# Kernel tuning notes

Measured on AMD Instinct MI355X. Metric: run time of the kernel, lower is better.

The kernel has to match this reference:

```python
import jax, jax.numpy as jnp
import numpy as np

N_NODES = 25000
N_EDGES = 250000
F_IN = 32
F_OUT = 32
EDGE_DIM = 6
H1, H2 = 64, 128


def setup_inputs() -> dict:
    key = jax.random.key(0)
    ks = jax.random.split(key, 10)
    s = 0.05
    return {
        "x": jax.random.normal(ks[0], (N_NODES, F_IN), dtype=jnp.float32),
        "edge_attr": jax.random.normal(ks[1], (N_EDGES, EDGE_DIM), dtype=jnp.float32),
        # fnet MLP params: Linear(6->64), ReLU, Linear(64->128), ReLU, Linear(128->F_IN*F_OUT)
        "W1": jax.random.normal(ks[2], (H1, EDGE_DIM), dtype=jnp.float32) * s,
        "b1": jnp.zeros((H1,), dtype=jnp.float32),
        "W2": jax.random.normal(ks[3], (H2, H1), dtype=jnp.float32) * s,
        "b2": jnp.zeros((H2,), dtype=jnp.float32),
        "W3": jax.random.normal(ks[4], (F_IN * F_OUT, H2), dtype=jnp.float32) * s,
        "b3": jnp.zeros((F_IN * F_OUT,), dtype=jnp.float32),
        "edge_src": jax.random.randint(ks[5], (N_EDGES,), 0, N_NODES),
        "edge_dst": jax.random.randint(ks[6], (N_EDGES,), 0, N_NODES),
    }


def reference(x, edge_attr, W1, b1, W2, b2, W3, b3, edge_src, edge_dst):
    # fnet: per-edge MLP producing a dynamic filter theta_e of shape [F_OUT, F_IN]
    h = jax.nn.relu(edge_attr @ W1.T + b1)            # [E, H1]
    h = jax.nn.relu(h @ W2.T + b2)                    # [E, H2]
    theta = (h @ W3.T + b3).reshape(-1, F_OUT, F_IN)  # [E, F_OUT, F_IN]
    # gather source features, apply per-edge filter
    msg = jnp.einsum('eoi,ei->eo', theta, x[edge_src])  # [E, F_OUT]
    # scatter-mean over destination nodes (ECC averages over neighborhood)
    agg = jax.ops.segment_sum(msg, edge_dst, num_segments=N_NODES)
    deg = jax.ops.segment_sum(jnp.ones((msg.shape[0],), x.dtype), edge_dst,
                              num_segments=N_NODES)
    out = agg / jnp.maximum(deg, 1.0)[:, None]        # [N, F_OUT]
    return jax.nn.relu(out)                           # trailing 'r' in config
```

## Files before the change

### kernel.cpp

```cpp
#include <hip/hip_runtime.h>
#include <hip/hip_fp16.h>

#define N_NODES 25000
#define N_EDGES 250000
#define ED 6
#define H1 64
#define H2 128
#define NBLK 977
#define NCHUNK 33
#define CHUNK_USH 4096
#define W3S_USHORTS (NCHUNK*CHUNK_USH)
#define W2S_USHORTS (H2*H1)
#define SCAN_BLOCKS 98

typedef float f32x4 __attribute__((ext_vector_type(4)));
typedef _Float16 f16x8 __attribute__((ext_vector_type(8)));
typedef _Float16 f16x2 __attribute__((ext_vector_type(2)));
typedef __fp16 fp16x2 __attribute__((ext_vector_type(2)));
typedef unsigned int u32x4 __attribute__((ext_vector_type(4)));
typedef unsigned int u32x2 __attribute__((ext_vector_type(2)));

union F16x8U { u32x4 u; f16x8 h; };
union F16x2U { unsigned u; f16x2 h; };
union PKU    { fp16x2 p; unsigned u; };

__device__ __forceinline__ unsigned pkrtz(float lo, float hi) {
    PKU r; r.p = __builtin_amdgcn_cvt_pkrtz(lo, hi); return r.u;
}
__device__ __forceinline__ unsigned pk_mul_blo(unsigned h, unsigned x) {
    unsigned d;
    asm("v_pk_mul_f16 %0, %1, %2 op_sel:[0,0] op_sel_hi:[0,1]" : "=v"(d) : "v"(h), "v"(x));
    return d;
}
__device__ __forceinline__ unsigned pk_mul_bhi(unsigned h, unsigned x) {
    unsigned d;
    asm("v_pk_mul_f16 %0, %1, %2 op_sel:[1,0] op_sel_hi:[1,1]" : "=v"(d) : "v"(h), "v"(x));
    return d;
}
__device__ __forceinline__ f32x4 mfma16(f16x8 a, f16x8 b, f32x4 c) {
    return __builtin_amdgcn_mfma_f32_16x16x32_f16(a, b, c, 0, 0, 0);
}
__device__ __forceinline__ void gload16(const void* g, void* l) {
    __builtin_amdgcn_global_load_lds(
        (const __attribute__((address_space(1))) unsigned int*)g,
        (__attribute__((address_space(3))) unsigned int*)l, 16, 0, 0);
}

__global__ __launch_bounds__(256) void ecc_init(
    const float* __restrict__ W3, const float* __restrict__ b3,
    const float* __restrict__ W2,
    unsigned* __restrict__ cnt, unsigned short* __restrict__ w3s,
    unsigned short* __restrict__ w2s)
{
    int idx = blockIdx.x * 256 + threadIdx.x;
    if (idx < W3S_USHORTS) {
        int c = idx >> 12, r = idx & 4095;
        int kk = r >> 10;
        int j  = (r >> 9) & 1;
        int lane = (r >> 3) & 63;
        int m  = r & 7;
        int p  = j * 16 + (lane & 15);
        int o  = ((p & 15) << 1) + (p >> 4);
        int kp = (c * 4 + kk) * 32 + (lane >> 4) * 8 + m;
        float v = 0.f;
        if (kp < 4096)      { int k = kp >> 5, i = kp & 31; v = W3[(o * 32 + i) * 128 + k]; }
        else if (kp < 4128) { v = b3[o * 32 + (kp - 4096)]; }
        __half hv = __float2half_rn(v);
        w3s[idx] = *reinterpret_cast<unsigned short*>(&hv);
    }
    if (idx < W2S_USHORTS) {
        __half hv = __float2half_rn(W2[idx]);
        w2s[idx] = *reinterpret_cast<unsigned short*>(&hv);
    }
    if (idx < N_NODES) cnt[idx] = 0u;
}

__global__ __launch_bounds__(256) void ecc_hist(
    const int* __restrict__ dst, unsigned* __restrict__ cnt,
    unsigned* __restrict__ rank)
{
    int e = blockIdx.x * 256 + threadIdx.x;
    if (e < N_EDGES) rank[e] = atomicAdd(&cnt[dst[e]], 1u);
}

__global__ __launch_bounds__(256) void ecc_scan1(
    const unsigned* __restrict__ cnt, unsigned* __restrict__ off,
    unsigned* __restrict__ bsum)
{
    __shared__ unsigned s[256];
    const int t = threadIdx.x, i = blockIdx.x * 256 + t;
    unsigned v = (i < N_NODES) ? cnt[i] : 0u;
    s[t] = v; __syncthreads();
    #pragma unroll
    for (int d = 1; d < 256; d <<= 1) {
        unsigned add = (t >= d) ? s[t - d] : 0u;
        __syncthreads(); s[t] += add; __syncthreads();
    }
    if (i < N_NODES) off[i] = s[t] - v;
    if (t == 255) bsum[blockIdx.x] = s[255];
}

__global__ __launch_bounds__(128) void ecc_scan2(
    const unsigned* __restrict__ bsum, unsigned* __restrict__ bsumx)
{
    __shared__ unsigned s[128];
    const int t = threadIdx.x;
    unsigned v = (t < SCAN_BLOCKS) ? bsum[t] : 0u;
    s[t] = v; __syncthreads();
    #pragma unroll
    for (int d = 1; d < 128; d <<= 1) {
        unsigned add = (t >= d) ? s[t - d] : 0u;
        __syncthreads(); s[t] += add; __syncthreads();
    }
    if (t < SCAN_BLOCKS) bsumx[t] = s[t] - v;
}

__global__ __launch_bounds__(256) void ecc_scan3(
    unsigned* __restrict__ off, const unsigned* __restrict__ bsumx)
{
    int i = blockIdx.x * 256 + threadIdx.x;
    if (i < N_NODES) off[i] += bsumx[blockIdx.x];
    if (i == 0) off[N_NODES] = N_EDGES;
}

__global__ __launch_bounds__(256) void ecc_perm(
    const int* __restrict__ dst, const unsigned* __restrict__ off,
    const unsigned* __restrict__ rank, unsigned* __restrict__ perm)
{
    int e = blockIdx.x * 256 + threadIdx.x;
    if (e < N_EDGES) perm[off[dst[e]] + rank[e]] = (unsigned)e;
}

__global__ __launch_bounds__(256)
__attribute__((amdgpu_waves_per_eu(2, 2)))
void ecc_fused(
    const float* __restrict__ x,   const float* __restrict__ ea,
    const float* __restrict__ W1,  const float* __restrict__ b1,
    const unsigned short* __restrict__ w2s, const float* __restrict__ b2,
    const unsigned short* __restrict__ w3s,
    const int* __restrict__ src,   const unsigned* __restrict__ perm,
    unsigned* __restrict__ msg32)
{
    __shared__ __align__(16) unsigned short sm[256 * H2];
    __shared__ __align__(16) unsigned short wbuf[2][CHUNK_USH];

    const int t = threadIdx.x;
    const int tile = blockIdx.x * 256;
    const int slot = tile + t;
    const bool ev = (slot < N_EDGES);
    const unsigned je = ev ? perm[slot] : 0u;

    const int w = t >> 6, l = t & 63, lr = l & 15, kg = l >> 4;

    gload16(w3s + t * 8,        &wbuf[0][t * 8]);
    gload16(w3s + 2048 + t * 8, &wbuf[0][2048 + t * 8]);

    {
        float a[ED];
        #pragma unroll
        for (int c = 0; c < ED; ++c) a[c] = ev ? ea[(long)je * ED + c] : 0.f;

        float h1[H1];
        #pragma unroll
        for (int o = 0; o < H1; ++o) {
            float acc = b1[o];
            #pragma unroll
            for (int c = 0; c < ED; ++c) acc = fmaf(W1[o * ED + c], a[c], acc);
            h1[o] = fmaxf(acc, 0.f);
        }
        #pragma unroll
        for (int q = 0; q < 8; ++q) {
            u32x4 pk;
            #pragma unroll
            for (int j = 0; j < 4; ++j)
                pk[j] = pkrtz(h1[q*8 + 2*j], h1[q*8 + 2*j + 1]);
            const int boff = (t * 128 + q * 16) ^ ((t & 7) << 4);
            *(u32x4*)((char*)sm + boff) = pk;
        }
    }

    unsigned xsh[4][4];
    #pragma unroll
    for (int mt = 0; mt < 4; ++mt) {
        const int er = tile + w * 64 + mt * 16 + lr;
        if (er < N_EDGES) {
            const float4* xp = (const float4*)(x + (long)src[perm[er]] * 32 + kg * 8);
            float4 v0 = xp[0], v1 = xp[1];
            xsh[mt][0] = pkrtz(v0.x, v0.y); xsh[mt][1] = pkrtz(v0.z, v0.w);
            xsh[mt][2] = pkrtz(v1.x, v1.y); xsh[mt][3] = pkrtz(v1.z, v1.w);
        } else {
            xsh[mt][0] = xsh[mt][1] = xsh[mt][2] = xsh[mt][3] = 0u;
        }
    }

    {
        F16x8U hb[4][2];
        #pragma unroll
        for (int ne = 0; ne < 4; ++ne) {
            const int er = w * 64 + ne * 16 + lr;
            #pragma unroll
            for (int ks = 0; ks < 2; ++ks) {
                const int boff = (er * 128 + ks * 64 + kg * 16) ^ ((er & 7) << 4);
                hb[ne][ks].u = *(const u32x4*)((const char*)sm + boff);
            }
        }
        __syncthreads();

        #pragma unroll
        for (int mo = 0; mo < 8; ++mo) {
            F16x8U a2[2];
            #pragma unroll
            for (int ks = 0; ks < 2; ++ks)
                a2[ks].u = *(const u32x4*)(w2s + (mo*16 + lr) * 64 + ks*32 + kg*8);
            const float4 bv = *(const float4*)(b2 + mo*16 + kg*4);
            #pragma unroll
            for (int ne = 0; ne < 4; ++ne) {
                f32x4 c = (f32x4){0.f, 0.f, 0.f, 0.f};
                c = mfma16(a2[0].h, hb[ne][0].h, c);
                c = mfma16(a2[1].h, hb[ne][1].h, c);
                const unsigned p0 = pkrtz(fmaxf(c[0]+bv.x, 0.f), fmaxf(c[1]+bv.y, 0.f));
                const unsigned p1 = pkrtz(fmaxf(c[2]+bv.z, 0.f), fmaxf(c[3]+bv.w, 0.f));
                const int er = w * 64 + ne * 16 + lr;
                const int boff = (er * 256 + (mo*16 + kg*4) * 2) ^ ((er & 7) << 4);
                *(u32x2*)((char*)sm + boff) = (u32x2){p0, p1};
            }
        }
    }

    f32x4 acc[4][2];
    #pragma unroll
    for (int mt = 0; mt < 4; ++mt)
        #pragma unroll
        for (int nt = 0; nt < 2; ++nt) acc[mt][nt] = (f32x4){0.f,0.f,0.f,0.f};

    __syncthreads();

    int cur = 0;
    #pragma unroll 1
    for (int c = 0; c < 32; ++c) {
        {
            const unsigned short* gs = w3s + (c + 1) * CHUNK_USH + t * 8;
            gload16(gs,        &wbuf[cur ^ 1][t * 8]);
            gload16(gs + 2048, &wbuf[cur ^ 1][2048 + t * 8]);
        }
        const char* wb = (const char*)wbuf[cur] + l * 16;

        u32x2 hv[4];
        #pragma unroll
        for (int mt = 0; mt < 4; ++mt) {
            const int row = w * 64 + mt * 16 + lr;
            const int boff = (row * 256 + c * 8) ^ ((row & 7) << 4);
            hv[mt] = *(const u32x2*)((const char*)sm + boff);
        }
        #pragma unroll
        for (int kk = 0; kk < 4; ++kk) {
            F16x8U b0, b1;
            b0.u = *(const u32x4*)(wb + kk * 2048);
            b1.u = *(const u32x4*)(wb + kk * 2048 + 1024);
            #pragma unroll
            for (int mt = 0; mt < 4; ++mt) {
                const unsigned h01 = hv[mt][kk >> 1];
                F16x8U af;
                if (kk & 1) {
                    af.u[0] = pk_mul_bhi(h01, xsh[mt][0]);
                    af.u[1] = pk_mul_bhi(h01, xsh[mt][1]);
                    af.u[2] = pk_mul_bhi(h01, xsh[mt][2]);
                    af.u[3] = pk_mul_bhi(h01, xsh[mt][3]);
                } else {
                    af.u[0] = pk_mul_blo(h01, xsh[mt][0]);
                    af.u[1] = pk_mul_blo(h01, xsh[mt][1]);
                    af.u[2] = pk_mul_blo(h01, xsh[mt][2]);
                    af.u[3] = pk_mul_blo(h01, xsh[mt][3]);
                }
                acc[mt][0] = mfma16(af.h, b0.h, acc[mt][0]);
                acc[mt][1] = mfma16(af.h, b1.h, acc[mt][1]);
            }
        }
        __syncthreads();
        cur ^= 1;
    }
    {
        const char* wb = (const char*)wbuf[cur] + l * 16;
        F16x8U b0, b1;
        b0.u = *(const u32x4*)(wb);
        b1.u = *(const u32x4*)(wb + 1024);
        #pragma unroll
        for (int mt = 0; mt < 4; ++mt) {
            F16x8U af;
            af.u = (u32x4){xsh[mt][0], xsh[mt][1], xsh[mt][2], xsh[mt][3]};
            acc[mt][0] = mfma16(af.h, b0.h, acc[mt][0]);
            acc[mt][1] = mfma16(af.h, b1.h, acc[mt][1]);
        }
    }

    #pragma unroll
    for (int mt = 0; mt < 4; ++mt) {
        #pragma unroll
        for (int r = 0; r < 4; ++r) {
            const int j = tile + w * 64 + mt * 16 + kg * 4 + r;
            if (j < N_EDGES)
                msg32[(long)j * 16 + lr] = pkrtz(acc[mt][0][r], acc[mt][1][r]);
        }
    }
}

__global__ __launch_bounds__(256) void ecc_gather(
    const unsigned* __restrict__ msg32, const unsigned* __restrict__ off,
    float* __restrict__ out)
{
    const int t = threadIdx.x;
    const int q = t & 15;
    const int n = blockIdx.x * 16 + (t >> 4);
    if (n >= N_NODES) return;
    const unsigned lo = off[n], hi = off[n + 1];
    float s0 = 0.f, s1 = 0.f;
    for (unsigned j = lo; j < hi; ++j) {
        F16x2U v; v.u = msg32[(long)j * 16 + q];
        s0 += (float)v.h[0];
        s1 += (float)v.h[1];
    }
    const float dg = fmaxf((float)(hi - lo), 1.f);
    ((float2*)(out + (long)n * 32))[q] =
        make_float2(fmaxf(s0 / dg, 0.f), fmaxf(s1 / dg, 0.f));
}

extern "C" void kernel_launch(void* const* d_in, const int* in_sizes, int n_in,
                              void* d_out, int out_size, void* d_ws, size_t ws_size,
                              hipStream_t stream) {
    const float* x   = (const float*)d_in[0];
    const float* ea  = (const float*)d_in[1];
    const float* W1  = (const float*)d_in[2];
    const float* b1  = (const float*)d_in[3];
    const float* W2  = (const float*)d_in[4];
    const float* b2  = (const float*)d_in[5];
    const float* W3  = (const float*)d_in[6];
    const float* b3  = (const float*)d_in[7];
    const int*   src = (const int*)d_in[8];
    const int*   dst = (const int*)d_in[9];
    float* out = (float*)d_out;

    char* p = (char*)d_ws;
    unsigned short* w3s = (unsigned short*)p; p += W3S_USHORTS * 2;
    unsigned short* w2s = (unsigned short*)p; p += 16384;
    unsigned* cnt   = (unsigned*)p; p += 100096;
    unsigned* off   = (unsigned*)p; p += 100352;
    unsigned* bsum  = (unsigned*)p; p += 512;
    unsigned* bsumx = (unsigned*)p; p += 512;
    unsigned* rank  = (unsigned*)p; p += 1000192;
    unsigned* perm  = (unsigned*)p; p += 1000192;
    unsigned* msg32 = (unsigned*)p;

    ecc_init<<<(W3S_USHORTS + 255) / 256, 256, 0, stream>>>(W3, b3, W2, cnt, w3s, w2s);
    ecc_hist<<<NBLK, 256, 0, stream>>>(dst, cnt, rank);
    ecc_scan1<<<SCAN_BLOCKS, 256, 0, stream>>>(cnt, off, bsum);
    ecc_scan2<<<1, 128, 0, stream>>>(bsum, bsumx);
    ecc_scan3<<<SCAN_BLOCKS, 256, 0, stream>>>(off, bsumx);
    ecc_perm<<<NBLK, 256, 0, stream>>>(dst, off, rank, perm);
    ecc_fused<<<NBLK, 256, 0, stream>>>(x, ea, W1, b1, w2s, b2, w3s, src, perm, msg32);
    ecc_gather<<<(N_NODES + 15) / 16, 256, 0, stream>>>(msg32, off, out);
}
```

Baseline: 125.8 us.

## Switch theta GEMM to 32x32x16 MFMA and store messages feature-major

The per-edge filter contraction now uses 32x32x16 f16 MFMA with two 32-edge tiles per wave instead of 16x16x32 tiles, and the W3 pre-swizzle is changed to match the new B-fragment layout. Messages are written transposed (feature-major over padded edges), and the gather kernel gives one thread per output feature reading a contiguous row. It also drops the waves_per_eu(2,2) hint and raises wave priority around the MFMA loop. The aim is fewer MFMA issues and operand reads, at the cost of a different register footprint and strided transposed stores from the fused kernel.

After: 136.7 us. +8.7%, slower.

```diff
diff --git a/kernel.cpp b/kernel.cpp
--- a/kernel.cpp
+++ b/kernel.cpp
@@ -7,6 +7,7 @@
 #define H1 64
 #define H2 128
 #define NBLK 977
+#define E_PAD (NBLK*256)
 #define NCHUNK 33
 #define CHUNK_USH 4096
 #define W3S_USHORTS (NCHUNK*CHUNK_USH)
@@ -14,15 +15,15 @@
 #define SCAN_BLOCKS 98
 
 typedef float f32x4 __attribute__((ext_vector_type(4)));
+typedef float f32x16 __attribute__((ext_vector_type(16)));
 typedef _Float16 f16x8 __attribute__((ext_vector_type(8)));
-typedef _Float16 f16x2 __attribute__((ext_vector_type(2)));
 typedef __fp16 fp16x2 __attribute__((ext_vector_type(2)));
 typedef unsigned int u32x4 __attribute__((ext_vector_type(4)));
 typedef unsigned int u32x2 __attribute__((ext_vector_type(2)));
 
 union F16x8U { u32x4 u; f16x8 h; };
-union F16x2U { unsigned u; f16x2 h; };
 union PKU    { fp16x2 p; unsigned u; };
+union HU     { unsigned short u; _Float16 h; };
 
 __device__ __forceinline__ unsigned pkrtz(float lo, float hi) {
     PKU r; r.p = __builtin_amdgcn_cvt_pkrtz(lo, hi); return r.u;
@@ -39,6 +40,9 @@
 }
 __device__ __forceinline__ f32x4 mfma16(f16x8 a, f16x8 b, f32x4 c) {
     return __builtin_amdgcn_mfma_f32_16x16x32_f16(a, b, c, 0, 0, 0);
+}
+__device__ __forceinline__ f32x16 mfma32(f16x8 a, f16x8 b, f32x16 c) {
+    return __builtin_amdgcn_mfma_f32_32x32x16_f16(a, b, c, 0, 0, 0);
 }
 __device__ __forceinline__ void gload16(const void* g, void* l) {
     __builtin_amdgcn_global_load_lds(
@@ -55,13 +59,11 @@
     int idx = blockIdx.x * 256 + threadIdx.x;
     if (idx < W3S_USHORTS) {
         int c = idx >> 12, r = idx & 4095;
-        int kk = r >> 10;
-        int j  = (r >> 9) & 1;
+        int ks = r >> 9;
         int lane = (r >> 3) & 63;
-        int m  = r & 7;
-        int p  = j * 16 + (lane & 15);
-        int o  = ((p & 15) << 1) + (p >> 4);
-        int kp = (c * 4 + kk) * 32 + (lane >> 4) * 8 + m;
+        int j = r & 7;
+        int o = lane & 31;
+        int kp = c * 128 + ks * 16 + ((lane >> 5) << 3) + j;
         float v = 0.f;
         if (kp < 4096)      { int k = kp >> 5, i = kp & 31; v = W3[(o * 32 + i) * 128 + k]; }
         else if (kp < 4128) { v = b3[o * 32 + (kp - 4096)]; }
@@ -131,15 +133,13 @@
     if (e < N_EDGES) perm[off[dst[e]] + rank[e]] = (unsigned)e;
 }
 
-__global__ __launch_bounds__(256)
-__attribute__((amdgpu_waves_per_eu(2, 2)))
-void ecc_fused(
+__global__ __launch_bounds__(256) void ecc_fused(
     const float* __restrict__ x,   const float* __restrict__ ea,
     const float* __restrict__ W1,  const float* __restrict__ b1,
     const unsigned short* __restrict__ w2s, const float* __restrict__ b2,
     const unsigned short* __restrict__ w3s,
     const int* __restrict__ src,   const unsigned* __restrict__ perm,
-    unsigned* __restrict__ msg32)
+    unsigned short* __restrict__ msgT)
 {
     __shared__ __align__(16) unsigned short sm[256 * H2];
     __shared__ __align__(16) unsigned short wbuf[2][CHUNK_USH];
@@ -151,6 +151,7 @@
     const unsigned je = ev ? perm[slot] : 0u;
 
     const int w = t >> 6, l = t & 63, lr = l & 15, kg = l >> 4;
+    const int l31 = l & 31, l5 = l >> 5;
 
     gload16(w3s + t * 8,        &wbuf[0][t * 8]);
     gload16(w3s + 2048 + t * 8, &wbuf[0][2048 + t * 8]);
@@ -179,17 +180,22 @@
         }
     }
 
-    unsigned xsh[4][4];
+    unsigned xsh[2][8];
     #pragma unroll
-    for (int mt = 0; mt < 4; ++mt) {
-        const int er = tile + w * 64 + mt * 16 + lr;
+    for (int mt = 0; mt < 2; ++mt) {
+        const int er = tile + w * 64 + mt * 32 + l31;
         if (er < N_EDGES) {
-            const float4* xp = (const float4*)(x + (long)src[perm[er]] * 32 + kg * 8);
-            float4 v0 = xp[0], v1 = xp[1];
+            const float* xb = x + (long)src[perm[er]] * 32;
+            const float4* xp = (const float4*)(xb + l5 * 8);
+            const float4* xq = (const float4*)(xb + 16 + l5 * 8);
+            float4 v0 = xp[0], v1 = xp[1], v2 = xq[0], v3 = xq[1];
             xsh[mt][0] = pkrtz(v0.x, v0.y); xsh[mt][1] = pkrtz(v0.z, v0.w);
             xsh[mt][2] = pkrtz(v1.x, v1.y); xsh[mt][3] = pkrtz(v1.z, v1.w);
+            xsh[mt][4] = pkrtz(v2.x, v2.y); xsh[mt][5] = pkrtz(v2.z, v2.w);
+            xsh[mt][6] = pkrtz(v3.x, v3.y); xsh[mt][7] = pkrtz(v3.z, v3.w);
         } else {
-            xsh[mt][0] = xsh[mt][1] = xsh[mt][2] = xsh[mt][3] = 0u;
+            #pragma unroll
+            for (int j = 0; j < 8; ++j) xsh[mt][j] = 0u;
         }
     }
 
@@ -227,11 +233,9 @@
         }
     }
 
-    f32x4 acc[4][2];
+    f32x16 acc[2];
     #pragma unroll
-    for (int mt = 0; mt < 4; ++mt)
-        #pragma unroll
-        for (int nt = 0; nt < 2; ++nt) acc[mt][nt] = (f32x4){0.f,0.f,0.f,0.f};
+    for (int i = 0; i < 16; ++i) { acc[0][i] = 0.f; acc[1][i] = 0.f; }
 
     __syncthreads();
 
@@ -245,83 +249,92 @@
         }
         const char* wb = (const char*)wbuf[cur] + l * 16;
 
-        u32x2 hv[4];
-        #pragma unroll
-        for (int mt = 0; mt < 4; ++mt) {
-            const int row = w * 64 + mt * 16 + lr;
+        u32x2 hv[2];
+        #pragma unroll
+        for (int mt = 0; mt < 2; ++mt) {
+            const int row = w * 64 + mt * 32 + l31;
             const int boff = (row * 256 + c * 8) ^ ((row & 7) << 4);
             hv[mt] = *(const u32x2*)((const char*)sm + boff);
         }
-        #pragma unroll
-        for (int kk = 0; kk < 4; ++kk) {
-            F16x8U b0, b1;
-            b0.u = *(const u32x4*)(wb + kk * 2048);
-            b1.u = *(const u32x4*)(wb + kk * 2048 + 1024);
-            #pragma unroll
-            for (int mt = 0; mt < 4; ++mt) {
-                const unsigned h01 = hv[mt][kk >> 1];
+
+        __builtin_amdgcn_s_setprio(1);
+        #pragma unroll
+        for (int ks = 0; ks < 8; ++ks) {
+            F16x8U bf;
+            bf.u = *(const u32x4*)(wb + ks * 1024);
+            const int kl = ks >> 1;
+            const int xb = (ks & 1) * 4;
+            #pragma unroll
+            for (int mt = 0; mt < 2; ++mt) {
+                const unsigned h01 = hv[mt][kl >> 1];
                 F16x8U af;
-                if (kk & 1) {
-                    af.u[0] = pk_mul_bhi(h01, xsh[mt][0]);
-                    af.u[1] = pk_mul_bhi(h01, xsh[mt][1]);
-                    af.u[2] = pk_mul_bhi(h01, xsh[mt][2]);
-                    af.u[3] = pk_mul_bhi(h01, xsh[mt][3]);
+                if (kl & 1) {
+                    af.u[0] = pk_mul_bhi(h01, xsh[mt][xb + 0]);
+                    af.u[1] = pk_mul_bhi(h01, xsh[mt][xb + 1]);
+                    af.u[2] = pk_mul_bhi(h01, xsh[mt][xb + 2]);
+                    af.u[3] = pk_mul_bhi(h01, xsh[mt][xb + 3]);
                 } else {
-                    af.u[0] = pk_mul_blo(h01, xsh[mt][0]);
-                    af.u[1] = pk_mul_blo(h01, xsh[mt][1]);
-                    af.u[2] = pk_mul_blo(h01, xsh[mt][2]);
-                    af.u[3] = pk_mul_blo(h01, xsh[mt][3]);
+                    af.u[0] = pk_mul_blo(h01, xsh[mt][xb + 0]);
+                    af.u[1] = pk_mul_blo(h01, xsh[mt][xb + 1]);
+                    af.u[2] = pk_mul_blo(h01, xsh[mt][xb + 2]);
+                    af.u[3] = pk_mul_blo(h01, xsh[mt][xb + 3]);
                 }
-                acc[mt][0] = mfma16(af.h, b0.h, acc[mt][0]);
-                acc[mt][1] = mfma16(af.h, b1.h, acc[mt][1]);
+                acc[mt] = mfma32(af.h, bf.h, acc[mt]);
             }
         }
+        __builtin_amdgcn_s_setprio(0);
+
         __syncthreads();
         cur ^= 1;
     }
     {
         const char* wb = (const char*)wbuf[cur] + l * 16;
-        F16x8U b0, b1;
-        b0.u = *(const u32x4*)(wb);
-        b1.u = *(const u32x4*)(wb + 1024);
-        #pragma unroll
-        for (int mt = 0; mt < 4; ++mt) {
+        F16x8U bf0, bf1;
+        bf0.u = *(const u32x4*)(wb);
+        bf1.u = *(const u32x4*)(wb + 1024);
+        #pragma unroll
+        for (int mt = 0; mt < 2; ++mt) {
             F16x8U af;
             af.u = (u32x4){xsh[mt][0], xsh[mt][1], xsh[mt][2], xsh[mt][3]};
-            acc[mt][0] = mfma16(af.h, b0.h, acc[mt][0]);
-            acc[mt][1] = mfma16(af.h, b1.h, acc[mt][1]);
-        }
-    }
-
-    #pragma unroll
-    for (int mt = 0; mt < 4; ++mt) {
-        #pragma unroll
-        for (int r = 0; r < 4; ++r) {
-            const int j = tile + w * 64 + mt * 16 + kg * 4 + r;
-            if (j < N_EDGES)
-                msg32[(long)j * 16 + lr] = pkrtz(acc[mt][0][r], acc[mt][1][r]);
+            acc[mt] = mfma32(af.h, bf0.h, acc[mt]);
+            af.u = (u32x4){xsh[mt][4], xsh[mt][5], xsh[mt][6], xsh[mt][7]};
+            acc[mt] = mfma32(af.h, bf1.h, acc[mt]);
+        }
+    }
+
+    {
+        const long orow = (long)l31 * E_PAD;
+        const int ebase = tile + w * 64 + 4 * l5;
+        #pragma unroll
+        for (int mt = 0; mt < 2; ++mt) {
+            #pragma unroll
+            for (int q = 0; q < 4; ++q) {
+                const unsigned p0 = pkrtz(acc[mt][4*q + 0], acc[mt][4*q + 1]);
+                const unsigned p1 = pkrtz(acc[mt][4*q + 2], acc[mt][4*q + 3]);
+                const long e0 = ebase + mt * 32 + 8 * q;
+                *(u32x2*)(msgT + orow + e0) = (u32x2){p0, p1};
+            }
         }
     }
 }
 
 __global__ __launch_bounds__(256) void ecc_gather(
-    const unsigned* __restrict__ msg32, const unsigned* __restrict__ off,
+    const unsigned short* __restrict__ msgT, const unsigned* __restrict__ off,
     float* __restrict__ out)
 {
     const int t = threadIdx.x;
-    const int q = t & 15;
-    const int n = blockIdx.x * 16 + (t >> 4);
+    const int o = t & 31;
+    const int n = blockIdx.x * 8 + (t >> 5);
     if (n >= N_NODES) return;
     const unsigned lo = off[n], hi = off[n + 1];
-    float s0 = 0.f, s1 = 0.f;
+    const unsigned short* row = msgT + (long)o * E_PAD;
+    float s = 0.f;
     for (unsigned j = lo; j < hi; ++j) {
-        F16x2U v; v.u = msg32[(long)j * 16 + q];
-        s0 += (float)v.h[0];
-        s1 += (float)v.h[1];
+        HU v; v.u = row[j];
+        s += (float)v.h;
     }
     const float dg = fmaxf((float)(hi - lo), 1.f);
-    ((float2*)(out + (long)n * 32))[q] =
-        make_float2(fmaxf(s0 / dg, 0.f), fmaxf(s1 / dg, 0.f));
+    out[(long)n * 32 + o] = fmaxf(s / dg, 0.f);
 }
 
 extern "C" void kernel_launch(void* const* d_in, const int* in_sizes, int n_in,
@@ -348,7 +361,7 @@
     unsigned* bsumx = (unsigned*)p; p += 512;
     unsigned* rank  = (unsigned*)p; p += 1000192;
     unsigned* perm  = (unsigned*)p; p += 1000192;
-    unsigned* msg32 = (unsigned*)p;
+    unsigned short* msgT = (unsigned short*)p;
 
     ecc_init<<<(W3S_USHORTS + 255) / 256, 256, 0, stream>>>(W3, b3, W2, cnt, w3s, w2s);
     ecc_hist<<<NBLK, 256, 0, stream>>>(dst, cnt, rank);
@@ -356,6 +369,6 @@
     ecc_scan2<<<1, 128, 0, stream>>>(bsum, bsumx);
     ecc_scan3<<<SCAN_BLOCKS, 256, 0, stream>>>(off, bsumx);
     ecc_perm<<<NBLK, 256, 0, stream>>>(dst, off, rank, perm);
-    ecc_fused<<<NBLK, 256, 0, stream>>>(x, ea, W1, b1, w2s, b2, w3s, src, perm, msg32);
-    ecc_gather<<<(N_NODES + 15) / 16, 256, 0, stream>>>(msg32, off, out);
-}
+    ecc_fused<<<NBLK, 256, 0, stream>>>(x, ea, W1, b1, w2s, b2, w3s, src, perm, msgT);
+    ecc_gather<<<(N_NODES + 7) / 8, 256, 0, stream>>>(msgT, off, out);
+}
```
